# Kernel tuning notes

Hardware: AMD Instinct MI355X
Metric: run time of the kernel (lower is better)

Reference implementation:

```python
import jax, jax.numpy as jnp
import numpy as np

N_A, N_B = 50000, 200000          # coarse / fine active voxel counts
C_A, C_B, C_OUT = 256, 128, 256   # channels: x_a, x_b (skip), output
K_T, M_T = 8, 100000              # transpose conv: 2^3 offsets, pairs per offset
K_C, M_C = 27, 120000             # 3x3x3 conv: 27 offsets, pairs per offset
EPS = 1e-5


def setup_inputs() -> dict:
    key = jax.random.key(0)
    ks = jax.random.split(key, 12)
    feats_a = jax.random.normal(ks[0], (N_A, C_A), jnp.float32)
    feats_b = jax.random.normal(ks[1], (N_B, C_B), jnp.float32)
    W_t = jax.random.normal(ks[2], (K_T, C_A, C_A), jnp.float32) * 0.05
    W_c = jax.random.normal(ks[3], (K_C, C_A + C_B, C_OUT), jnp.float32) * 0.05
    in_map_t = jax.random.randint(ks[4], (K_T, M_T), 0, N_A, dtype=jnp.int32)
    out_map_t = jax.random.randint(ks[5], (K_T, M_T), 0, N_B, dtype=jnp.int32)
    in_map_c = jax.random.randint(ks[6], (K_C, M_C), 0, N_B, dtype=jnp.int32)
    out_map_c = jax.random.randint(ks[7], (K_C, M_C), 0, N_B, dtype=jnp.int32)
    bn_t_gamma = jax.random.uniform(ks[8], (C_A,), jnp.float32, 0.5, 1.5)
    bn_t_beta = jax.random.normal(ks[9], (C_A,), jnp.float32) * 0.1
    bn_t_mean = jax.random.normal(ks[10], (C_A,), jnp.float32) * 0.1
    bn_t_var = jax.random.uniform(ks[11], (C_A,), jnp.float32, 0.5, 1.5)
    k2 = jax.random.split(jax.random.key(1), 4)
    bn_c_gamma = jax.random.uniform(k2[0], (C_OUT,), jnp.float32, 0.5, 1.5)
    bn_c_beta = jax.random.normal(k2[1], (C_OUT,), jnp.float32) * 0.1
    bn_c_mean = jax.random.normal(k2[2], (C_OUT,), jnp.float32) * 0.1
    bn_c_var = jax.random.uniform(k2[3], (C_OUT,), jnp.float32, 0.5, 1.5)
    return {
        "feats_a": feats_a, "feats_b": feats_b,
        "W_t": W_t, "bn_t_gamma": bn_t_gamma, "bn_t_beta": bn_t_beta,
        "bn_t_mean": bn_t_mean, "bn_t_var": bn_t_var,
        "W_c": W_c, "bn_c_gamma": bn_c_gamma, "bn_c_beta": bn_c_beta,
        "bn_c_mean": bn_c_mean, "bn_c_var": bn_c_var,
        "in_map_t": in_map_t, "out_map_t": out_map_t,
        "in_map_c": in_map_c, "out_map_c": out_map_c,
    }


def _sparse_conv(feats, in_map, out_map, W, n_out):
    """MinkowskiEngine gather-GEMM-scatter over kernel maps.
    feats: [N_in, C_in]; in_map/out_map: [K, M] index pairs per kernel offset;
    W: [K, C_in, C_out]. Scan over the K offsets (small fixed set) to keep
    peak memory at one [M, C] slab."""
    acc0 = jnp.zeros((n_out, W.shape[-1]), feats.dtype)

    def step(acc, kmaps):
        im, om, Wk = kmaps
        acc = acc.at[om].add(feats[im] @ Wk)  # gather -> GEMM -> scatter-add
        return acc, None

    out, _ = jax.lax.scan(step, acc0, (in_map, out_map, W))
    return out


def _bn_relu(x, gamma, beta, mean, var):
    # BatchNorm in eval mode (running stats) + ReLU
    return jax.nn.relu((x - mean) * (gamma / jnp.sqrt(var + EPS)) + beta)


def reference(feats_a, feats_b, W_t, bn_t_gamma, bn_t_beta, bn_t_mean, bn_t_var,
              W_c, bn_c_gamma, bn_c_beta, bn_c_mean, bn_c_var,
              in_map_t, out_map_t, in_map_c, out_map_c):
    # conv_a: transpose conv (k=2, s=2) -> BN -> ReLU; output lives on x_b coords
    xa = _sparse_conv(feats_a, in_map_t, out_map_t, W_t, N_B)
    xa = _bn_relu(xa, bn_t_gamma, bn_t_beta, bn_t_mean, bn_t_var)
    # ME.cat: concatenate features at identical coordinates
    x = jnp.concatenate([xa, feats_b], axis=-1)  # [N_B, C_A + C_B]
    # conv_proj: 3x3x3 conv -> BN -> ReLU
    x = _sparse_conv(x, in_map_c, out_map_c, W_c, N_B)
    return _bn_relu(x, bn_c_gamma, bn_c_beta, bn_c_mean, bn_c_var)
```

## Files before the change

### kernel.cpp

```cpp
#include <hip/hip_runtime.h>
#include <hip/hip_bf16.h>
#include <stdint.h>

typedef __attribute__((ext_vector_type(8))) short bf16x8;
typedef __attribute__((ext_vector_type(4))) float floatx4;

#define DEV __device__ __forceinline__

DEV void gl_lds16(const void* g, void* lds) {
    __builtin_amdgcn_global_load_lds(
        (const __attribute__((address_space(1))) unsigned int*)g,
        (__attribute__((address_space(3))) unsigned int*)lds, 16, 0, 0);
}

struct __align__(8) bf4 { __hip_bfloat16 h[4]; };

template <int KSTEPS>
__global__ __launch_bounds__(256) void spconv_stage1(
    const __hip_bfloat16* __restrict__ A, const __hip_bfloat16* __restrict__ BT,
    const int* __restrict__ in_map, __hip_bfloat16* __restrict__ P, int M) {
    constexpr int K = KSTEPS * 32;
    __shared__ __align__(16) char Abuf[8192];
    __shared__ __align__(16) char Bbuf[8192];

    const int tid = threadIdx.x;
    const int w = tid >> 6;
    const int l = tid & 63;
    const int kz = blockIdx.z;
    const int m0 = blockIdx.x * 128;
    const int n0 = blockIdx.y * 128;

    const int* im = in_map + (size_t)kz * M;

    const int rS = (w & 1) * 64 + l;
    int prow = m0 + rS;
    if (prow > M - 1) prow = M - 1;
    const __hip_bfloat16* a_row = A + (size_t)im[prow] * K;
    const __hip_bfloat16* b_row = BT + ((size_t)kz * 256 + n0 + rS) * (size_t)K;
    const int q0 = w >> 1;

    char* Al = Abuf + w * 1024 + l * 16;
    char* Bl = Bbuf + w * 1024 + l * 16;

    floatx4 acc[4][4];
#pragma unroll
    for (int i = 0; i < 4; i++)
#pragma unroll
        for (int j = 0; j < 4; j++) acc[i][j] = (floatx4)0.0f;

    const int wm = w & 1, wn = w >> 1;
    const int lm = l & 15, lq = l >> 4;

    for (int ks = 0; ks < KSTEPS; ks++) {
        const int kb = ks * 32;
        gl_lds16(a_row + kb + q0 * 8, Al);
        gl_lds16(a_row + kb + (q0 + 2) * 8, Al + 4096);
        gl_lds16(b_row + kb + q0 * 8, Bl);
        gl_lds16(b_row + kb + (q0 + 2) * 8, Bl + 4096);
        __syncthreads();

        bf16x8 af[4], bf[4];
#pragma unroll
        for (int mt = 0; mt < 4; mt++)
            af[mt] = *(const bf16x8*)(Abuf + lq * 2048 + (wm * 64 + mt * 16 + lm) * 16);
#pragma unroll
        for (int nt = 0; nt < 4; nt++)
            bf[nt] = *(const bf16x8*)(Bbuf + lq * 2048 + (wn * 64 + nt * 16 + lm) * 16);

#pragma unroll
        for (int mt = 0; mt < 4; mt++)
#pragma unroll
            for (int nt = 0; nt < 4; nt++)
                acc[mt][nt] = __builtin_amdgcn_mfma_f32_16x16x32_bf16(
                    af[mt], bf[nt], acc[mt][nt], 0, 0, 0);

        __syncthreads();
    }

    __hip_bfloat16* pbase = P + (size_t)kz * M * 256 + n0 + wn * 64 + lm * 4;
#pragma unroll
    for (int mt = 0; mt < 4; mt++) {
        const int rowb = wm * 64 + mt * 16 + lq * 4;
#pragma unroll
        for (int r = 0; r < 4; r++) {
            const int pair = m0 + rowb + r;
            if (pair < M) {
                bf4 o;
#pragma unroll
                for (int nt = 0; nt < 4; nt++)
                    o.h[nt] = __float2bfloat16(acc[mt][nt][r]);
                *(bf4*)(pbase + (size_t)pair * 256) = o;
            }
        }
    }
}

__global__ void stage2_kernel(const unsigned* __restrict__ start,
                              const unsigned* __restrict__ entries,
                              const __hip_bfloat16* __restrict__ P,
                              int kp_lo, int kp_hi,
                              float* __restrict__ partial, int init, int fin_mode,
                              __hip_bfloat16* __restrict__ xbf,
                              float* __restrict__ outp,
                              const float* __restrict__ g, const float* __restrict__ b,
                              const float* __restrict__ mu, const float* __restrict__ var) {
    const int tid = threadIdx.x;
    const int r = blockIdx.x * 4 + (tid >> 6);
    const int l = tid & 63;
    const int pos0 = l * 4;

    float acc[4];
    if (init) {
        acc[0] = acc[1] = acc[2] = acc[3] = 0.0f;
    } else {
        const float4 t = *(const float4*)(partial + (size_t)r * 256 + pos0);
        acc[0] = t.x; acc[1] = t.y; acc[2] = t.z; acc[3] = t.w;
    }

    const unsigned s0 = start[r], s1 = start[r + 1];
    for (unsigned e = s0; e < s1; ++e) {
        const int kp = (int)entries[e];
        if (kp >= kp_lo && kp < kp_hi) {
            const bf4 v = *(const bf4*)(P + (size_t)(kp - kp_lo) * 256 + pos0);
#pragma unroll
            for (int j = 0; j < 4; j++) acc[j] += __bfloat162float(v.h[j]);
        }
    }

    if (fin_mode == 0) {
        *(float4*)(partial + (size_t)r * 256 + pos0) =
            make_float4(acc[0], acc[1], acc[2], acc[3]);
    } else {
        const int chunk = l >> 4, lm = l & 15;
#pragma unroll
        for (int j = 0; j < 4; j++) {
            const int c = chunk * 64 + j * 16 + lm;
            const float s = g[c] * rsqrtf(var[c] + 1e-5f);
            const float val = fmaxf((acc[j] - mu[c]) * s + b[c], 0.0f);
            if (fin_mode == 1)
                xbf[(size_t)r * 384 + c] = __float2bfloat16(val);
            else
                outp[(size_t)r * 256 + c] = val;
        }
    }
}

__global__ void hist_kernel(const int* __restrict__ om, int n,
                            unsigned* __restrict__ cnt) {
    int stride = gridDim.x * blockDim.x;
    for (int i = blockIdx.x * blockDim.x + threadIdx.x; i < n; i += stride)
        atomicAdd(&cnt[om[i]], 1u);
}

__global__ void scan1_kernel(const unsigned* __restrict__ cnt,
                             unsigned* __restrict__ start,
                             unsigned* __restrict__ bsum, int N) {
    __shared__ unsigned sums[256];
    const int t = threadIdx.x;
    const int base = blockIdx.x * 1024 + t * 4;
    unsigned v[4];
#pragma unroll
    for (int j = 0; j < 4; j++) v[j] = (base + j < N) ? cnt[base + j] : 0u;
    const unsigned T = v[0] + v[1] + v[2] + v[3];
    sums[t] = T;
    __syncthreads();
    for (int off = 1; off < 256; off <<= 1) {
        unsigned x = (t >= off) ? sums[t - off] : 0u;
        __syncthreads();
        sums[t] += x;
        __syncthreads();
    }
    unsigned run = sums[t] - T;
#pragma unroll
    for (int j = 0; j < 4; j++) {
        if (base + j < N) start[base + j] = run;
        run += v[j];
    }
    if (t == 255) bsum[blockIdx.x] = sums[255];
}

__global__ void scan2_kernel(unsigned* bsum, int nb) {
    __shared__ unsigned sums[256];
    const int t = threadIdx.x;
    const unsigned v = (t < nb) ? bsum[t] : 0u;
    sums[t] = v;
    __syncthreads();
    for (int off = 1; off < 256; off <<= 1) {
        unsigned x = (t >= off) ? sums[t - off] : 0u;
        __syncthreads();
        sums[t] += x;
        __syncthreads();
    }
    if (t < nb) bsum[t] = sums[t] - v;
}

__global__ void scan3_kernel(unsigned* __restrict__ start,
                             const unsigned* __restrict__ bsum,
                             unsigned* __restrict__ cursor, int N, unsigned total) {
    const int t = threadIdx.x;
    const int base = blockIdx.x * 1024 + t * 4;
    const unsigned add = bsum[blockIdx.x];
#pragma unroll
    for (int j = 0; j < 4; j++) {
        const int i = base + j;
        if (i < N) {
            const unsigned s = start[i] + add;
            start[i] = s;
            cursor[i] = s;
        }
    }
    if (blockIdx.x == gridDim.x - 1 && t == 255) start[N] = total;
}

__global__ void scatter_kernel(const int* __restrict__ om, int n,
                               unsigned* __restrict__ cursor,
                               unsigned* __restrict__ entries) {
    int stride = gridDim.x * blockDim.x;
    for (int i = blockIdx.x * blockDim.x + threadIdx.x; i < n; i += stride) {
        unsigned pos = atomicAdd(&cursor[om[i]], 1u);
        entries[pos] = (unsigned)i;
    }
}

__global__ void cast_bf16_kernel(const float* __restrict__ in,
                                 __hip_bfloat16* __restrict__ out, int n4) {
    int stride = gridDim.x * blockDim.x;
    for (int i = blockIdx.x * blockDim.x + threadIdx.x; i < n4; i += stride) {
        float4 v = ((const float4*)in)[i];
        bf4 o;
        o.h[0] = __float2bfloat16(v.x);
        o.h[1] = __float2bfloat16(v.y);
        o.h[2] = __float2bfloat16(v.z);
        o.h[3] = __float2bfloat16(v.w);
        ((bf4*)out)[i] = o;
    }
}

__global__ void transpose_cast_w(const float* __restrict__ W,
                                 __hip_bfloat16* __restrict__ WT, int Koff,
                                 int Cin, int Cout) {
    int total = Koff * Cin * Cout;
    int stride = gridDim.x * blockDim.x;
    for (int i = blockIdx.x * blockDim.x + threadIdx.x; i < total; i += stride) {
        int k = i / (Cin * Cout);
        int r = i - k * (Cin * Cout);
        int n = r / Cin;
        int kk = r - n * Cin;
        WT[i] = __float2bfloat16(W[((size_t)k * Cin + kk) * Cout + n]);
    }
}

__global__ void concat_b_kernel(const float* __restrict__ fb,
                                __hip_bfloat16* __restrict__ X) {
    const int total = 200000 * 32;
    int stride = gridDim.x * blockDim.x;
    for (int i = blockIdx.x * blockDim.x + threadIdx.x; i < total; i += stride) {
        int row = i >> 5;
        int c4 = (i & 31) * 4;
        float4 t = *(const float4*)(fb + (size_t)row * 128 + c4);
        bf4 o;
        o.h[0] = __float2bfloat16(t.x);
        o.h[1] = __float2bfloat16(t.y);
        o.h[2] = __float2bfloat16(t.z);
        o.h[3] = __float2bfloat16(t.w);
        *(bf4*)(X + (size_t)row * 384 + 256 + c4) = o;
    }
}

template <int KSTEPS>
__global__ __launch_bounds__(256) void spconv_atomic(
    const __hip_bfloat16* __restrict__ A, const __hip_bfloat16* __restrict__ BT,
    const int* __restrict__ in_map, const int* __restrict__ out_map,
    float* __restrict__ Out, int M) {
    constexpr int K = KSTEPS * 32;
    __shared__ __align__(16) char Abuf[8192];
    __shared__ __align__(16) char Bbuf[8192];
    __shared__ int om_s[128];

    const int tid = threadIdx.x;
    const int w = tid >> 6;
    const int l = tid & 63;
    const int koff = blockIdx.z;
    const int m0 = blockIdx.x * 128;
    const int n0 = blockIdx.y * 128;

    const int* im = in_map + (size_t)koff * M;
    const int* om = out_map + (size_t)koff * M;

    if (tid < 128) {
        int p = m0 + tid;
        om_s[tid] = (p < M) ? om[p] : -1;
    }

    const int rS = (w & 1) * 64 + l;
    int prow = m0 + rS;
    if (prow > M - 1) prow = M - 1;
    const __hip_bfloat16* a_row = A + (size_t)im[prow] * K;
    const __hip_bfloat16* b_row = BT + ((size_t)koff * 256 + n0 + rS) * (size_t)K;
    const int q0 = w >> 1;

    char* Al = Abuf + w * 1024 + l * 16;
    char* Bl = Bbuf + w * 1024 + l * 16;

    floatx4 acc[4][4];
#pragma unroll
    for (int i = 0; i < 4; i++)
#pragma unroll
        for (int j = 0; j < 4; j++) acc[i][j] = (floatx4)0.0f;

    const int wm = w & 1, wn = w >> 1;
    const int lm = l & 15, lq = l >> 4;

    for (int ks = 0; ks < KSTEPS; ks++) {
        const int kb = ks * 32;
        gl_lds16(a_row + kb + q0 * 8, Al);
        gl_lds16(a_row + kb + (q0 + 2) * 8, Al + 4096);
        gl_lds16(b_row + kb + q0 * 8, Bl);
        gl_lds16(b_row + kb + (q0 + 2) * 8, Bl + 4096);
        __syncthreads();

        bf16x8 af[4], bf[4];
#pragma unroll
        for (int mt = 0; mt < 4; mt++)
            af[mt] = *(const bf16x8*)(Abuf + lq * 2048 + (wm * 64 + mt * 16 + lm) * 16);
#pragma unroll
        for (int nt = 0; nt < 4; nt++)
            bf[nt] = *(const bf16x8*)(Bbuf + lq * 2048 + (wn * 64 + nt * 16 + lm) * 16);

#pragma unroll
        for (int mt = 0; mt < 4; mt++)
#pragma unroll
            for (int nt = 0; nt < 4; nt++)
                acc[mt][nt] = __builtin_amdgcn_mfma_f32_16x16x32_bf16(
                    af[mt], bf[nt], acc[mt][nt], 0, 0, 0);

        __syncthreads();
    }

#pragma unroll
    for (int mt = 0; mt < 4; mt++) {
        const int mbase = wm * 64 + mt * 16 + lq * 4;
#pragma unroll
        for (int r = 0; r < 4; r++) {
            const int orow = om_s[mbase + r];
            if (orow >= 0) {
                float* dst = Out + (size_t)orow * 256 + n0 + wn * 64 + lm;
#pragma unroll
                for (int nt = 0; nt < 4; nt++)
                    unsafeAtomicAdd(dst + nt * 16, acc[mt][nt][r]);
            }
        }
    }
}

__global__ void bn_concat_kernel(const float* __restrict__ xa,
                                 const float* __restrict__ fb,
                                 const float* __restrict__ g,
                                 const float* __restrict__ b,
                                 const float* __restrict__ mu,
                                 const float* __restrict__ var,
                                 __hip_bfloat16* __restrict__ X) {
    const int total = 200000 * 96;
    int stride = gridDim.x * blockDim.x;
    for (int i = blockIdx.x * blockDim.x + threadIdx.x; i < total; i += stride) {
        int row = i / 96;
        int c4 = (i - row * 96) * 4;
        float v[4];
        if (c4 < 256) {
            float4 t = *(const float4*)(xa + (size_t)row * 256 + c4);
            v[0] = t.x; v[1] = t.y; v[2] = t.z; v[3] = t.w;
#pragma unroll
            for (int j = 0; j < 4; j++) {
                int c = c4 + j;
                float s = g[c] * rsqrtf(var[c] + 1e-5f);
                v[j] = fmaxf((v[j] - mu[c]) * s + b[c], 0.0f);
            }
        } else {
            float4 t = *(const float4*)(fb + (size_t)row * 128 + (c4 - 256));
            v[0] = t.x; v[1] = t.y; v[2] = t.z; v[3] = t.w;
        }
        bf4 o;
#pragma unroll
        for (int j = 0; j < 4; j++) o.h[j] = __float2bfloat16(v[j]);
        *(bf4*)(X + (size_t)row * 384 + c4) = o;
    }
}

__global__ void bn_out_kernel(float* __restrict__ out, const float* __restrict__ g,
                              const float* __restrict__ b,
                              const float* __restrict__ mu,
                              const float* __restrict__ var) {
    const int total = 200000 * 64;
    int stride = gridDim.x * blockDim.x;
    for (int i = blockIdx.x * blockDim.x + threadIdx.x; i < total; i += stride) {
        int c4 = (i & 63) * 4;
        float4 t = ((const float4*)out)[i];
        float v[4] = {t.x, t.y, t.z, t.w};
#pragma unroll
        for (int j = 0; j < 4; j++) {
            int c = c4 + j;
            float s = g[c] * rsqrtf(var[c] + 1e-5f);
            v[j] = fmaxf((v[j] - mu[c]) * s + b[c], 0.0f);
        }
        ((float4*)out)[i] = make_float4(v[0], v[1], v[2], v[3]);
    }
}

extern "C" void kernel_launch(void* const* d_in, const int* in_sizes, int n_in,
                              void* d_out, int out_size, void* d_ws,
                              size_t ws_size, hipStream_t stream) {
    const float* feats_a = (const float*)d_in[0];
    const float* feats_b = (const float*)d_in[1];
    const float* W_t = (const float*)d_in[2];
    const float* bn_t_gamma = (const float*)d_in[3];
    const float* bn_t_beta = (const float*)d_in[4];
    const float* bn_t_mean = (const float*)d_in[5];
    const float* bn_t_var = (const float*)d_in[6];
    const float* W_c = (const float*)d_in[7];
    const float* bn_c_gamma = (const float*)d_in[8];
    const float* bn_c_beta = (const float*)d_in[9];
    const float* bn_c_mean = (const float*)d_in[10];
    const float* bn_c_var = (const float*)d_in[11];
    const int* in_map_t = (const int*)d_in[12];
    const int* out_map_t = (const int*)d_in[13];
    const int* in_map_c = (const int*)d_in[14];
    const int* out_map_c = (const int*)d_in[15];
    float* out = (float*)d_out;

    char* ws = (char*)d_ws;
    __hip_bfloat16* a_bf = (__hip_bfloat16*)(ws + 0);
    __hip_bfloat16* wtT  = (__hip_bfloat16*)(ws + 25600000);
    __hip_bfloat16* wcT  = (__hip_bfloat16*)(ws + 26648576);
    __hip_bfloat16* x_bf = (__hip_bfloat16*)(ws + 31956992);
    unsigned* cnt   = (unsigned*)(ws + 185556992);
    unsigned* start = (unsigned*)(ws + 186356992);
    unsigned* bsum  = (unsigned*)(ws + 187157248);
    unsigned* cur   = (unsigned*)(ws + 187158272);
    unsigned* ent   = (unsigned*)(ws + 187958272);
    __hip_bfloat16* P = (__hip_bfloat16*)(ws + 200918272);
    const size_t p_avail = (ws_size > 200918272u) ? ws_size - 200918272u : 0;
    int g_c = (int)(p_avail / 61440000ull); if (g_c > 27) g_c = 27;
    int g_t = (int)(p_avail / 51200000ull); if (g_t > 8) g_t = 8;
    const bool ts_t = (g_t >= 4);
    const bool ts_c = (g_c >= 5);

    cast_bf16_kernel<<<512, 256, 0, stream>>>(feats_a, a_bf, 50000 * 256 / 4);
    transpose_cast_w<<<512, 256, 0, stream>>>(W_t, wtT, 8, 256, 256);
    transpose_cast_w<<<512, 256, 0, stream>>>(W_c, wcT, 27, 384, 256);

    if (ts_t) {
        concat_b_kernel<<<2048, 256, 0, stream>>>(feats_b, x_bf);
        hipMemsetAsync(cnt, 0, 800000, stream);
        hist_kernel<<<1024, 256, 0, stream>>>(out_map_t, 800000, cnt);
        scan1_kernel<<<196, 256, 0, stream>>>(cnt, start, bsum, 200000);
        scan2_kernel<<<1, 256, 0, stream>>>(bsum, 196);
        scan3_kernel<<<196, 256, 0, stream>>>(start, bsum, cur, 200000, 800000);
        scatter_kernel<<<1024, 256, 0, stream>>>(out_map_t, 800000, cur, ent);
        for (int q0 = 0; q0 < 8; q0 += g_t) {
            const int q1 = (q0 + g_t < 8) ? q0 + g_t : 8;
            dim3 gs(782, 2, q1 - q0);
            spconv_stage1<8><<<gs, 256, 0, stream>>>(
                a_bf, wtT + (size_t)q0 * 256 * 256, in_map_t + (size_t)q0 * 100000,
                P, 100000);
            stage2_kernel<<<50000, 256, 0, stream>>>(
                start, ent, P, q0 * 100000, q1 * 100000, out, (q0 == 0) ? 1 : 0,
                (q1 == 8) ? 1 : 0, x_bf, out, bn_t_gamma, bn_t_beta, bn_t_mean,
                bn_t_var);
        }
    } else {
        hipMemsetAsync(d_out, 0, (size_t)out_size * sizeof(float), stream);
        dim3 g1(782, 2, 8);
        spconv_atomic<8><<<g1, 256, 0, stream>>>(a_bf, wtT, in_map_t, out_map_t,
                                                 out, 100000);
        bn_concat_kernel<<<2048, 256, 0, stream>>>(out, feats_b, bn_t_gamma,
                                                   bn_t_beta, bn_t_mean, bn_t_var,
                                                   x_bf);
    }

    if (ts_c) {
        hipMemsetAsync(cnt, 0, 800000, stream);
        hist_kernel<<<1024, 256, 0, stream>>>(out_map_c, 3240000, cnt);
        scan1_kernel<<<196, 256, 0, stream>>>(cnt, start, bsum, 200000);
        scan2_kernel<<<1, 256, 0, stream>>>(bsum, 196);
        scan3_kernel<<<196, 256, 0, stream>>>(start, bsum, cur, 200000, 3240000);
        scatter_kernel<<<1024, 256, 0, stream>>>(out_map_c, 3240000, cur, ent);
        for (int q0 = 0; q0 < 27; q0 += g_c) {
            const int q1 = (q0 + g_c < 27) ? q0 + g_c : 27;
            dim3 gs(938, 2, q1 - q0);
            spconv_stage1<12><<<gs, 256, 0, stream>>>(
                x_bf, wcT + (size_t)q0 * 256 * 384, in_map_c + (size_t)q0 * 120000,
                P, 120000);
            stage2_kernel<<<50000, 256, 0, stream>>>(
                start, ent, P, q0 * 120000, q1 * 120000, out, (q0 == 0) ? 1 : 0,
                (q1 == 27) ? 2 : 0, x_bf, out, bn_c_gamma, bn_c_beta, bn_c_mean,
                bn_c_var);
        }
    } else {
        hipMemsetAsync(d_out, 0, (size_t)out_size * sizeof(float), stream);
        dim3 g2(938, 2, 27);
        spconv_atomic<12><<<g2, 256, 0, stream>>>(x_bf, wcT, in_map_c, out_map_c,
                                                  out, 120000);
        bn_out_kernel<<<2048, 256, 0, stream>>>(out, bn_c_gamma, bn_c_beta,
                                                bn_c_mean, bn_c_var);
    }
}
```

Baseline: 4.130 ms.

## Load GEMM fragments directly to registers with double buffering; batch scatter gathers

The gather-GEMM kernel no longer stages A and B tiles through LDS with barriers. Each lane loads its MFMA fragments straight from global memory into registers and prefetches the next k-step while the current one computes. The scatter/reduce kernel now issues four gathered loads per iteration, masking invalid entries with a zero weight, to raise memory-level parallelism. In exchange, the GEMM does more redundant global loads because fragments are no longer shared through LDS, it uses more registers, and masked entries still cost a dummy load.

```diff
diff --git a/kernel.cpp b/kernel.cpp
--- a/kernel.cpp
+++ b/kernel.cpp
@@ -20,27 +20,28 @@
     const __hip_bfloat16* __restrict__ A, const __hip_bfloat16* __restrict__ BT,
     const int* __restrict__ in_map, __hip_bfloat16* __restrict__ P, int M) {
     constexpr int K = KSTEPS * 32;
-    __shared__ __align__(16) char Abuf[8192];
-    __shared__ __align__(16) char Bbuf[8192];
-
     const int tid = threadIdx.x;
     const int w = tid >> 6;
     const int l = tid & 63;
+    const int wm = w & 1, wn = w >> 1;
+    const int lm = l & 15, lq = l >> 4;
     const int kz = blockIdx.z;
     const int m0 = blockIdx.x * 128;
     const int n0 = blockIdx.y * 128;
 
     const int* im = in_map + (size_t)kz * M;
 
-    const int rS = (w & 1) * 64 + l;
-    int prow = m0 + rS;
-    if (prow > M - 1) prow = M - 1;
-    const __hip_bfloat16* a_row = A + (size_t)im[prow] * K;
-    const __hip_bfloat16* b_row = BT + ((size_t)kz * 256 + n0 + rS) * (size_t)K;
-    const int q0 = w >> 1;
-
-    char* Al = Abuf + w * 1024 + l * 16;
-    char* Bl = Bbuf + w * 1024 + l * 16;
+    const __hip_bfloat16* arow[4];
+#pragma unroll
+    for (int mt = 0; mt < 4; mt++) {
+        int p = m0 + wm * 64 + mt * 16 + lm;
+        if (p > M - 1) p = M - 1;
+        arow[mt] = A + (size_t)im[p] * K + lq * 8;
+    }
+    const __hip_bfloat16* brow[4];
+#pragma unroll
+    for (int nt = 0; nt < 4; nt++)
+        brow[nt] = BT + ((size_t)kz * 256 + n0 + wn * 64 + nt * 16 + lm) * (size_t)K + lq * 8;
 
     floatx4 acc[4][4];
 #pragma unroll
@@ -48,33 +49,29 @@
 #pragma unroll
         for (int j = 0; j < 4; j++) acc[i][j] = (floatx4)0.0f;
 
-    const int wm = w & 1, wn = w >> 1;
-    const int lm = l & 15, lq = l >> 4;
-
+    bf16x8 af[2][4], bf[2][4];
+#pragma unroll
+    for (int i = 0; i < 4; i++) {
+        af[0][i] = *(const bf16x8*)(arow[i]);
+        bf[0][i] = *(const bf16x8*)(brow[i]);
+    }
+
+#pragma unroll
     for (int ks = 0; ks < KSTEPS; ks++) {
-        const int kb = ks * 32;
-        gl_lds16(a_row + kb + q0 * 8, Al);
-        gl_lds16(a_row + kb + (q0 + 2) * 8, Al + 4096);
-        gl_lds16(b_row + kb + q0 * 8, Bl);
-        gl_lds16(b_row + kb + (q0 + 2) * 8, Bl + 4096);
-        __syncthreads();
-
-        bf16x8 af[4], bf[4];
-#pragma unroll
-        for (int mt = 0; mt < 4; mt++)
-            af[mt] = *(const bf16x8*)(Abuf + lq * 2048 + (wm * 64 + mt * 16 + lm) * 16);
-#pragma unroll
-        for (int nt = 0; nt < 4; nt++)
-            bf[nt] = *(const bf16x8*)(Bbuf + lq * 2048 + (wn * 64 + nt * 16 + lm) * 16);
-
+        const int cur = ks & 1, nxt = cur ^ 1;
+        if (ks + 1 < KSTEPS) {
+#pragma unroll
+            for (int i = 0; i < 4; i++) {
+                af[nxt][i] = *(const bf16x8*)(arow[i] + (ks + 1) * 32);
+                bf[nxt][i] = *(const bf16x8*)(brow[i] + (ks + 1) * 32);
+            }
+        }
 #pragma unroll
         for (int mt = 0; mt < 4; mt++)
 #pragma unroll
             for (int nt = 0; nt < 4; nt++)
                 acc[mt][nt] = __builtin_amdgcn_mfma_f32_16x16x32_bf16(
-                    af[mt], bf[nt], acc[mt][nt], 0, 0, 0);
-
-        __syncthreads();
+                    af[cur][mt], bf[cur][nt], acc[mt][nt], 0, 0, 0);
     }
 
     __hip_bfloat16* pbase = P + (size_t)kz * M * 256 + n0 + wn * 64 + lm * 4;
@@ -118,13 +115,27 @@
     }
 
     const unsigned s0 = start[r], s1 = start[r + 1];
-    for (unsigned e = s0; e < s1; ++e) {
-        const int kp = (int)entries[e];
-        if (kp >= kp_lo && kp < kp_hi) {
-            const bf4 v = *(const bf4*)(P + (size_t)(kp - kp_lo) * 256 + pos0);
-#pragma unroll
-            for (int j = 0; j < 4; j++) acc[j] += __bfloat162float(v.h[j]);
-        }
+    const unsigned cnt = s1 - s0;
+    for (unsigned i = 0; i < cnt; i += 4) {
+        const bf4* addr[4];
+        float wgt[4];
+#pragma unroll
+        for (int j = 0; j < 4; j++) {
+            unsigned idx = i + j;
+            unsigned ee = s0 + ((idx < cnt) ? idx : (cnt - 1));
+            const int kp = (int)entries[ee];
+            const bool ok = (idx < cnt) & (kp >= kp_lo) & (kp < kp_hi);
+            addr[j] = (const bf4*)(P + (ok ? (size_t)(kp - kp_lo) * 256 : 0) + pos0);
+            wgt[j] = ok ? 1.0f : 0.0f;
+        }
+        bf4 v[4];
+#pragma unroll
+        for (int j = 0; j < 4; j++) v[j] = *addr[j];
+#pragma unroll
+        for (int j = 0; j < 4; j++)
+#pragma unroll
+            for (int c = 0; c < 4; c++)
+                acc[c] = fmaf(wgt[j], __bfloat162float(v[j].h[c]), acc[c]);
     }
 
     if (fin_mode == 0) {
```

New measurement: 4.932 ms. 19.4% more time.
